# Performance work log

Hardware: AMD Instinct MI355X
Metric: run time of the kernel (lower is better)

Reference implementation:

```python
import jax, jax.numpy as jnp
import numpy as np
import math

B, S, D_MODEL, N_HEAD = 4, 2048, 1024, 16
D_K = D_MODEL // N_HEAD
ROPE_THETA = 10000.0


def _rope(x):
    # x: [B, H, S, Dk]; interleaved-pair rotary embedding.
    b, h, s, d = x.shape
    inv_freq = ROPE_THETA ** (-jnp.arange(0, d, 2, dtype=jnp.float32) / d)  # [d/2]
    ang = jnp.arange(s, dtype=jnp.float32)[:, None] * inv_freq[None, :]      # [S, d/2]
    cos, sin = jnp.cos(ang), jnp.sin(ang)
    x1, x2 = x[..., 0::2], x[..., 1::2]
    r1 = x1 * cos - x2 * sin
    r2 = x1 * sin + x2 * cos
    return jnp.stack([r1, r2], axis=-1).reshape(b, h, s, d)


def setup_inputs() -> dict:
    key = jax.random.key(0)
    ks = jax.random.split(key, 7)
    sc = 1.0 / math.sqrt(D_MODEL)
    return {
        "q": jax.random.normal(ks[0], (B, S, D_MODEL), jnp.float32),
        "k": jax.random.normal(ks[1], (B, S, D_MODEL), jnp.float32),
        "v": jax.random.normal(ks[2], (B, S, D_MODEL), jnp.float32),
        "Wq": jax.random.normal(ks[3], (D_MODEL, D_MODEL), jnp.float32) * sc,
        "Wk": jax.random.normal(ks[4], (D_MODEL, D_MODEL), jnp.float32) * sc,
        "Wv": jax.random.normal(ks[5], (D_MODEL, D_MODEL), jnp.float32) * sc,
        "Wo": jax.random.normal(ks[6], (D_MODEL, D_MODEL), jnp.float32) * sc,
    }


def _split(x):
    b, s, d = x.shape
    return x.reshape(b, s, N_HEAD, d // N_HEAD).transpose(0, 2, 1, 3)  # [B,H,S,Dk]


def reference(q, k, v, Wq, Wk, Wv, Wo):
    q = jnp.einsum("bsd,de->bse", q, Wq)
    k = jnp.einsum("bsd,de->bse", k, Wk)
    v = jnp.einsum("bsd,de->bse", v, Wv)
    qh, kh, vh = _split(q), _split(k), _split(v)
    qh, kh = _rope(qh), _rope(kh)
    scale = 1.0 / math.sqrt(D_K)
    score = jnp.einsum("bhqd,bhkd->bhqk", qh, kh) * scale  # [B,H,S,S]
    attn = jax.nn.softmax(score, axis=-1)
    out = jnp.einsum("bhqk,bhkd->bhqd", attn, vh)
    out = out.transpose(0, 2, 1, 3).reshape(q.shape[0], q.shape[1], D_MODEL)
    return jnp.einsum("bsd,de->bse", out, Wo)
```

## Files before the change

kernel.cpp:

```cpp
#include <hip/hip_runtime.h>
#include <stdint.h>

#define Bv 4
#define Sv 2048
#define Dv 1024
#define Hv 16
#define DKv 64
#define BSv (Bv * Sv)

typedef unsigned short u16;
typedef __attribute__((ext_vector_type(8))) short short8;
typedef __attribute__((ext_vector_type(8))) unsigned short u16x8;
typedef __attribute__((ext_vector_type(4))) unsigned short u16x4;
typedef __attribute__((ext_vector_type(4))) float f32x4;

__device__ __forceinline__ u16 f2bf(float f) {
  union { float f; uint32_t u; } x; x.f = f;
  uint32_t r = x.u + 0x7FFFu + ((x.u >> 16) & 1u);
  return (u16)(r >> 16);
}

__device__ __forceinline__ void gl_lds16(const void* g, void* l) {
  __builtin_amdgcn_global_load_lds(
      (__attribute__((address_space(1))) void*)g,
      (__attribute__((address_space(3))) void*)l, 16, 0, 0);
}

__device__ __forceinline__ f32x4 mfma16(short8 a, short8 b, f32x4 c) {
  return __builtin_amdgcn_mfma_f32_16x16x32_bf16(a, b, c, 0, 0, 0);
}

__global__ __launch_bounds__(256) void conv_qkv(
    const float* __restrict__ q, const float* __restrict__ k,
    const float* __restrict__ v, u16* __restrict__ qb, u16* __restrict__ kb,
    u16* __restrict__ vb) {
  const float* src = (blockIdx.y == 0) ? q : (blockIdx.y == 1 ? k : v);
  u16* dst = (blockIdx.y == 0) ? qb : (blockIdx.y == 1 ? kb : vb);
  int i = (blockIdx.x * 256 + threadIdx.x) * 8;
  const float4* s4 = (const float4*)(src + i);
  float4 a = s4[0], b = s4[1];
  u16x8 o = { f2bf(a.x), f2bf(a.y), f2bf(a.z), f2bf(a.w),
              f2bf(b.x), f2bf(b.y), f2bf(b.z), f2bf(b.w) };
  *(u16x8*)(dst + i) = o;
}

__global__ __launch_bounds__(256) void conv_wt(
    const float* __restrict__ w0, const float* __restrict__ w1,
    const float* __restrict__ w2, const float* __restrict__ w3,
    u16* __restrict__ t0, u16* __restrict__ t1, u16* __restrict__ t2,
    u16* __restrict__ t3) {
  const float* W = (blockIdx.z == 0) ? w0 : (blockIdx.z == 1 ? w1 : (blockIdx.z == 2 ? w2 : w3));
  u16* T = (blockIdx.z == 0) ? t0 : (blockIdx.z == 1 ? t1 : (blockIdx.z == 2 ? t2 : t3));
  __shared__ u16 tile[64][72];
  int nb = blockIdx.x * 64, kb = blockIdx.y * 64;
  int t = threadIdx.x;
#pragma unroll
  for (int p = 0; p < 4; ++p) {
    int idx = p * 256 + t;
    int r = idx >> 4;
    int c4 = (idx & 15) * 4;
    float4 vv = *(const float4*)(W + (size_t)(kb + r) * Dv + nb + c4);
    tile[c4 + 0][r] = f2bf(vv.x);
    tile[c4 + 1][r] = f2bf(vv.y);
    tile[c4 + 2][r] = f2bf(vv.z);
    tile[c4 + 3][r] = f2bf(vv.w);
  }
  __syncthreads();
#pragma unroll
  for (int p = 0; p < 4; ++p) {
    int idx = p * 256 + t;
    int r = idx >> 4;
    int c4 = (idx & 15) * 4;
    u16x4 o = { tile[r][c4], tile[r][c4 + 1], tile[r][c4 + 2], tile[r][c4 + 3] };
    *(u16x4*)(T + (size_t)(nb + r) * Dv + kb + c4) = o;
  }
}

__global__ __launch_bounds__(256) void gemm_bt(
    const u16* __restrict__ A, const u16* __restrict__ Bt,
    void* __restrict__ Out, int mode) {
  __shared__ u16 As[128 * 64];
  __shared__ u16 Bs[128 * 64];
  int tid = threadIdx.x;
  int lane = tid & 63, wid = tid >> 6;
  int quad = lane >> 4, cc = lane & 15;
  int wm = (wid >> 1) * 64, wn = (wid & 1) * 64;
  int m0 = blockIdx.x * 128, n0 = blockIdx.y * 128;

  f32x4 acc[4][4];
#pragma unroll
  for (int mi = 0; mi < 4; ++mi)
#pragma unroll
    for (int ni = 0; ni < 4; ++ni) {
      f32x4 z = {0.f, 0.f, 0.f, 0.f};
      acc[mi][ni] = z;
    }

  for (int k0 = 0; k0 < Dv; k0 += 64) {
#pragma unroll
    for (int p = 0; p < 4; ++p) {
      int slot = p * 256 + tid;
      int row = slot >> 3, cl = slot & 7;
      int cg = cl ^ (row & 7);
      gl_lds16(A + (size_t)(m0 + row) * Dv + k0 + cg * 8, &As[slot * 8]);
    }
#pragma unroll
    for (int p = 0; p < 4; ++p) {
      int slot = p * 256 + tid;
      int row = slot >> 3, cl = slot & 7;
      int cg = cl ^ (row & 7);
      gl_lds16(Bt + (size_t)(n0 + row) * Dv + k0 + cg * 8, &Bs[slot * 8]);
    }
    __syncthreads();
#pragma unroll
    for (int kk = 0; kk < 2; ++kk) {
      short8 af[4], bf[4];
#pragma unroll
      for (int mi = 0; mi < 4; ++mi) {
        int row = wm + mi * 16 + cc;
        int cg = kk * 4 + quad;
        af[mi] = *(const short8*)&As[row * 64 + (cg ^ (row & 7)) * 8];
      }
#pragma unroll
      for (int ni = 0; ni < 4; ++ni) {
        int row = wn + ni * 16 + cc;
        int cg = kk * 4 + quad;
        bf[ni] = *(const short8*)&Bs[row * 64 + (cg ^ (row & 7)) * 8];
      }
#pragma unroll
      for (int mi = 0; mi < 4; ++mi)
#pragma unroll
        for (int ni = 0; ni < 4; ++ni)
          acc[mi][ni] = mfma16(af[mi], bf[ni], acc[mi][ni]);
    }
    __syncthreads();
  }

  if (mode <= 1) {
    u16* O = (u16*)Out;
    float postscale = (mode == 0) ? 0.125f : 1.0f;
#pragma unroll
    for (int ni = 0; ni < 4; ++ni) {
      int n = n0 + wn + ni * 16 + cc;
      int h = n >> 6, d = n & 63;
      float inv = __expf(-(float)(d & 62) * (9.210340372f / 64.0f));
      float sign = (d & 1) ? 1.0f : -1.0f;
#pragma unroll
      for (int mi = 0; mi < 4; ++mi) {
        int mB = m0 + wm + mi * 16 + quad * 4;
#pragma unroll
        for (int r = 0; r < 4; ++r) {
          int m = mB + r;
          int b = m >> 11, s = m & (Sv - 1);
          float val = acc[mi][ni][r];
          float part = __shfl_xor(val, 1);
          float sn, cs;
          __sincosf((float)s * inv, &sn, &cs);
          float outv = (val * cs + sign * part * sn) * postscale;
          O[((size_t)(b * Hv + h) * Sv + s) * DKv + d] = f2bf(outv);
        }
      }
    }
  } else if (mode == 2) {
    u16* O = (u16*)Out;
#pragma unroll
    for (int ni = 0; ni < 4; ++ni) {
      int n = n0 + wn + ni * 16 + cc;
      int h = n >> 6, d = n & 63;
#pragma unroll
      for (int mi = 0; mi < 4; ++mi) {
        int mB = m0 + wm + mi * 16 + quad * 4;
        int b = mB >> 11, s = mB & (Sv - 1);
        u16x4 o4 = { f2bf(acc[mi][ni][0]), f2bf(acc[mi][ni][1]),
                     f2bf(acc[mi][ni][2]), f2bf(acc[mi][ni][3]) };
        *(u16x4*)&O[((size_t)(b * Hv + h) * DKv + d) * Sv + s] = o4;
      }
    }
  } else {
    float* O = (float*)Out;
#pragma unroll
    for (int ni = 0; ni < 4; ++ni) {
      int n = n0 + wn + ni * 16 + cc;
#pragma unroll
      for (int mi = 0; mi < 4; ++mi) {
        int mB = m0 + wm + mi * 16 + quad * 4;
#pragma unroll
        for (int r = 0; r < 4; ++r)
          O[(size_t)(mB + r) * Dv + n] = acc[mi][ni][r];
      }
    }
  }
}

__global__ __launch_bounds__(256) void attn(
    const u16* __restrict__ Qp, const u16* __restrict__ Kp,
    const u16* __restrict__ Vt, u16* __restrict__ ctx) {
  __shared__ u16 Ks[2][64 * 64];
  __shared__ u16 Vs[2][64 * 64];
  __shared__ u16 Ps[4][32 * 72];
  int tid = threadIdx.x;
  int lane = tid & 63, wid = tid >> 6;
  int quad = lane >> 4, cc = lane & 15;
  int bh = blockIdx.y;
  int q0 = blockIdx.x * 128 + wid * 32;
  const u16* Qh = Qp + (size_t)bh * Sv * DKv;
  const u16* Kh = Kp + (size_t)bh * Sv * DKv;
  const u16* Vh = Vt + (size_t)bh * Sv * DKv;

  short8 qf[2][2];
#pragma unroll
  for (int mi = 0; mi < 2; ++mi)
#pragma unroll
    for (int kk = 0; kk < 2; ++kk)
      qf[mi][kk] = *(const short8*)&Qh[(size_t)(q0 + mi * 16 + cc) * DKv + kk * 32 + quad * 8];

  f32x4 o[2][4];
  float lacc[2][4];
#pragma unroll
  for (int mi = 0; mi < 2; ++mi) {
#pragma unroll
    for (int nd = 0; nd < 4; ++nd) {
      f32x4 z = {0.f, 0.f, 0.f, 0.f};
      o[mi][nd] = z;
    }
#pragma unroll
    for (int r = 0; r < 4; ++r) lacc[mi][r] = 0.f;
  }

#pragma unroll
  for (int p = 0; p < 2; ++p) {
    int slot = p * 256 + tid;
    int row = slot >> 3, cl = slot & 7;
    int cg = cl ^ (row & 7);
    gl_lds16(Kh + (size_t)row * DKv + cg * 8, &Ks[0][slot * 8]);
    gl_lds16(Vh + (size_t)row * Sv + cg * 8, &Vs[0][slot * 8]);
  }

  for (int kt = 0; kt < Sv / 64; ++kt) {
    int cur = kt & 1;
    __syncthreads();

    if (kt + 1 < Sv / 64) {
      int s1 = (kt + 1) * 64;
#pragma unroll
      for (int p = 0; p < 2; ++p) {
        int slot = p * 256 + tid;
        int row = slot >> 3, cl = slot & 7;
        int cg = cl ^ (row & 7);
        gl_lds16(Kh + (size_t)(s1 + row) * DKv + cg * 8, &Ks[1 - cur][slot * 8]);
        gl_lds16(Vh + (size_t)row * Sv + s1 + cg * 8, &Vs[1 - cur][slot * 8]);
      }
    }

    f32x4 sc[2][4];
#pragma unroll
    for (int mi = 0; mi < 2; ++mi)
#pragma unroll
      for (int kc = 0; kc < 4; ++kc) {
        f32x4 z = {0.f, 0.f, 0.f, 0.f};
        sc[mi][kc] = z;
      }
#pragma unroll
    for (int kk = 0; kk < 2; ++kk) {
      short8 kf[4];
#pragma unroll
      for (int kc = 0; kc < 4; ++kc) {
        int row = kc * 16 + cc;
        int cg = kk * 4 + quad;
        kf[kc] = *(const short8*)&Ks[cur][row * 64 + (cg ^ (row & 7)) * 8];
      }
#pragma unroll
      for (int mi = 0; mi < 2; ++mi)
#pragma unroll
        for (int kc = 0; kc < 4; ++kc)
          sc[mi][kc] = mfma16(qf[mi][kk], kf[kc], sc[mi][kc]);
    }

#pragma unroll
    for (int mi = 0; mi < 2; ++mi)
#pragma unroll
      for (int kc = 0; kc < 4; ++kc)
#pragma unroll
        for (int r = 0; r < 4; ++r) {
          float pv = __expf(sc[mi][kc][r]);
          uint32_t u = __float_as_uint(pv);
          lacc[mi][r] += __uint_as_float(u & 0xFFFF0000u);
          Ps[wid][(mi * 16 + quad * 4 + r) * 72 + kc * 16 + cc] = (u16)(u >> 16);
        }

#pragma unroll
    for (int kk = 0; kk < 2; ++kk) {
      short8 pf[2], vf[4];
#pragma unroll
      for (int mi = 0; mi < 2; ++mi)
        pf[mi] = *(const short8*)&Ps[wid][(mi * 16 + cc) * 72 + (kk * 4 + quad) * 8];
#pragma unroll
      for (int nd = 0; nd < 4; ++nd) {
        int row = nd * 16 + cc;
        int cg = kk * 4 + quad;
        vf[nd] = *(const short8*)&Vs[cur][row * 64 + (cg ^ (row & 7)) * 8];
      }
#pragma unroll
      for (int mi = 0; mi < 2; ++mi)
#pragma unroll
        for (int nd = 0; nd < 4; ++nd)
          o[mi][nd] = mfma16(pf[mi], vf[nd], o[mi][nd]);
    }
  }

#pragma unroll
  for (int mi = 0; mi < 2; ++mi)
#pragma unroll
    for (int r = 0; r < 4; ++r) {
      float l = lacc[mi][r];
#pragma unroll
      for (int off = 1; off < 16; off <<= 1)
        l += __shfl_xor(l, off);
      lacc[mi][r] = 1.0f / l;
    }

  int b = bh >> 4, h = bh & 15;
#pragma unroll
  for (int mi = 0; mi < 2; ++mi)
#pragma unroll
    for (int r = 0; r < 4; ++r) {
      int s = q0 + mi * 16 + quad * 4 + r;
      float linv = lacc[mi][r];
#pragma unroll
      for (int nd = 0; nd < 4; ++nd) {
        int d = h * DKv + nd * 16 + cc;
        ctx[((size_t)b * Sv + s) * Dv + d] = f2bf(o[mi][nd][r] * linv);
      }
    }
}

extern "C" void kernel_launch(void* const* d_in, const int* in_sizes, int n_in,
                              void* d_out, int out_size, void* d_ws, size_t ws_size,
                              hipStream_t stream) {
  (void)in_sizes; (void)n_in; (void)out_size; (void)ws_size;
  const float* q  = (const float*)d_in[0];
  const float* k  = (const float*)d_in[1];
  const float* v  = (const float*)d_in[2];
  const float* Wq = (const float*)d_in[3];
  const float* Wk = (const float*)d_in[4];
  const float* Wv = (const float*)d_in[5];
  const float* Wo = (const float*)d_in[6];

  char* ws = (char*)d_ws;
  size_t off = 0;
  const size_t big = (size_t)BSv * Dv * sizeof(u16);
  const size_t wsz = (size_t)Dv * Dv * sizeof(u16);
  u16* qb  = (u16*)(ws + off); off += big;
  u16* kb  = (u16*)(ws + off); off += big;
  u16* vb  = (u16*)(ws + off); off += big;
  u16* Wqt = (u16*)(ws + off); off += wsz;
  u16* Wkt = (u16*)(ws + off); off += wsz;
  u16* Wvt = (u16*)(ws + off); off += wsz;
  u16* Wot = (u16*)(ws + off); off += wsz;
  u16* Qp  = (u16*)(ws + off); off += big;
  u16* Kp  = (u16*)(ws + off); off += big;
  u16* Vtr = (u16*)(ws + off); off += big;
  u16* ctx = (u16*)(ws + off); off += big;

  conv_qkv<<<dim3(BSv * Dv / (256 * 8), 3), 256, 0, stream>>>(q, k, v, qb, kb, vb);
  conv_wt<<<dim3(Dv / 64, Dv / 64, 4), 256, 0, stream>>>(Wq, Wk, Wv, Wo, Wqt, Wkt, Wvt, Wot);
  gemm_bt<<<dim3(BSv / 128, Dv / 128), 256, 0, stream>>>(qb, Wqt, Qp, 0);
  gemm_bt<<<dim3(BSv / 128, Dv / 128), 256, 0, stream>>>(kb, Wkt, Kp, 1);
  gemm_bt<<<dim3(BSv / 128, Dv / 128), 256, 0, stream>>>(vb, Wvt, Vtr, 2);
  attn<<<dim3(Sv / 128, Bv * Hv), 256, 0, stream>>>(Qp, Kp, Vtr, ctx);
  gemm_bt<<<dim3(BSv / 128, Dv / 128), 256, 0, stream>>>(ctx, Wot, d_out, 3);
}
```

Baseline: 371.1 us.

## Double attention query tile per wave, use exp2 and MFMA row-sum

```diff
diff --git a/kernel.cpp b/kernel.cpp
--- a/kernel.cpp
+++ b/kernel.cpp
@@ -138,7 +138,7 @@
 
   if (mode <= 1) {
     u16* O = (u16*)Out;
-    float postscale = (mode == 0) ? 0.125f : 1.0f;
+    float postscale = (mode == 0) ? 0.18033688011112042f : 1.0f;
 #pragma unroll
     for (int ni = 0; ni < 4; ++ni) {
       int n = n0 + wn + ni * 16 + cc;
@@ -197,34 +197,37 @@
     const u16* __restrict__ Vt, u16* __restrict__ ctx) {
   __shared__ u16 Ks[2][64 * 64];
   __shared__ u16 Vs[2][64 * 64];
-  __shared__ u16 Ps[4][32 * 72];
+  __shared__ u16 Ps[4][64 * 72];
   int tid = threadIdx.x;
   int lane = tid & 63, wid = tid >> 6;
   int quad = lane >> 4, cc = lane & 15;
   int bh = blockIdx.y;
-  int q0 = blockIdx.x * 128 + wid * 32;
+  int q0 = blockIdx.x * 256 + wid * 64;
   const u16* Qh = Qp + (size_t)bh * Sv * DKv;
   const u16* Kh = Kp + (size_t)bh * Sv * DKv;
   const u16* Vh = Vt + (size_t)bh * Sv * DKv;
 
-  short8 qf[2][2];
-#pragma unroll
-  for (int mi = 0; mi < 2; ++mi)
+  const short8 ones = { (short)0x3F80, (short)0x3F80, (short)0x3F80, (short)0x3F80,
+                        (short)0x3F80, (short)0x3F80, (short)0x3F80, (short)0x3F80 };
+
+  short8 qf[4][2];
+#pragma unroll
+  for (int mi = 0; mi < 4; ++mi)
 #pragma unroll
     for (int kk = 0; kk < 2; ++kk)
       qf[mi][kk] = *(const short8*)&Qh[(size_t)(q0 + mi * 16 + cc) * DKv + kk * 32 + quad * 8];
 
-  f32x4 o[2][4];
-  float lacc[2][4];
-#pragma unroll
-  for (int mi = 0; mi < 2; ++mi) {
+  f32x4 o[4][4];
+  f32x4 ol[4];
+#pragma unroll
+  for (int mi = 0; mi < 4; ++mi) {
 #pragma unroll
     for (int nd = 0; nd < 4; ++nd) {
       f32x4 z = {0.f, 0.f, 0.f, 0.f};
       o[mi][nd] = z;
     }
-#pragma unroll
-    for (int r = 0; r < 4; ++r) lacc[mi][r] = 0.f;
+    f32x4 z = {0.f, 0.f, 0.f, 0.f};
+    ol[mi] = z;
   }
 
 #pragma unroll
@@ -252,48 +255,42 @@
       }
     }
 
-    f32x4 sc[2][4];
-#pragma unroll
-    for (int mi = 0; mi < 2; ++mi)
+    short8 kf[4][2];
+#pragma unroll
+    for (int kc = 0; kc < 4; ++kc)
+#pragma unroll
+      for (int kk = 0; kk < 2; ++kk) {
+        int row = kc * 16 + cc;
+        int cg = kk * 4 + quad;
+        kf[kc][kk] = *(const short8*)&Ks[cur][row * 64 + (cg ^ (row & 7)) * 8];
+      }
+
+#pragma unroll
+    for (int mi = 0; mi < 4; ++mi) {
+      f32x4 sc[4];
 #pragma unroll
       for (int kc = 0; kc < 4; ++kc) {
         f32x4 z = {0.f, 0.f, 0.f, 0.f};
-        sc[mi][kc] = z;
-      }
+        sc[kc] = z;
+      }
+#pragma unroll
+      for (int kk = 0; kk < 2; ++kk)
+#pragma unroll
+        for (int kc = 0; kc < 4; ++kc)
+          sc[kc] = mfma16(qf[mi][kk], kf[kc][kk], sc[kc]);
+#pragma unroll
+      for (int kc = 0; kc < 4; ++kc)
+#pragma unroll
+        for (int r = 0; r < 4; ++r) {
+          float pv = __builtin_amdgcn_exp2f(sc[kc][r]);
+          Ps[wid][(mi * 16 + quad * 4 + r) * 72 + kc * 16 + cc] =
+              (u16)(__float_as_uint(pv) >> 16);
+        }
+    }
+
 #pragma unroll
     for (int kk = 0; kk < 2; ++kk) {
-      short8 kf[4];
-#pragma unroll
-      for (int kc = 0; kc < 4; ++kc) {
-        int row = kc * 16 + cc;
-        int cg = kk * 4 + quad;
-        kf[kc] = *(const short8*)&Ks[cur][row * 64 + (cg ^ (row & 7)) * 8];
-      }
-#pragma unroll
-      for (int mi = 0; mi < 2; ++mi)
-#pragma unroll
-        for (int kc = 0; kc < 4; ++kc)
-          sc[mi][kc] = mfma16(qf[mi][kk], kf[kc], sc[mi][kc]);
-    }
-
-#pragma unroll
-    for (int mi = 0; mi < 2; ++mi)
-#pragma unroll
-      for (int kc = 0; kc < 4; ++kc)
-#pragma unroll
-        for (int r = 0; r < 4; ++r) {
-          float pv = __expf(sc[mi][kc][r]);
-          uint32_t u = __float_as_uint(pv);
-          lacc[mi][r] += __uint_as_float(u & 0xFFFF0000u);
-          Ps[wid][(mi * 16 + quad * 4 + r) * 72 + kc * 16 + cc] = (u16)(u >> 16);
-        }
-
-#pragma unroll
-    for (int kk = 0; kk < 2; ++kk) {
-      short8 pf[2], vf[4];
-#pragma unroll
-      for (int mi = 0; mi < 2; ++mi)
-        pf[mi] = *(const short8*)&Ps[wid][(mi * 16 + cc) * 72 + (kk * 4 + quad) * 8];
+      short8 vf[4], pf[4];
 #pragma unroll
       for (int nd = 0; nd < 4; ++nd) {
         int row = nd * 16 + cc;
@@ -301,31 +298,26 @@
         vf[nd] = *(const short8*)&Vs[cur][row * 64 + (cg ^ (row & 7)) * 8];
       }
 #pragma unroll
-      for (int mi = 0; mi < 2; ++mi)
+      for (int mi = 0; mi < 4; ++mi)
+        pf[mi] = *(const short8*)&Ps[wid][(mi * 16 + cc) * 72 + (kk * 4 + quad) * 8];
+#pragma unroll
+      for (int mi = 0; mi < 4; ++mi)
+        ol[mi] = mfma16(pf[mi], ones, ol[mi]);
+#pragma unroll
+      for (int mi = 0; mi < 4; ++mi)
 #pragma unroll
         for (int nd = 0; nd < 4; ++nd)
           o[mi][nd] = mfma16(pf[mi], vf[nd], o[mi][nd]);
     }
   }
 
-#pragma unroll
-  for (int mi = 0; mi < 2; ++mi)
-#pragma unroll
-    for (int r = 0; r < 4; ++r) {
-      float l = lacc[mi][r];
-#pragma unroll
-      for (int off = 1; off < 16; off <<= 1)
-        l += __shfl_xor(l, off);
-      lacc[mi][r] = 1.0f / l;
-    }
-
   int b = bh >> 4, h = bh & 15;
 #pragma unroll
-  for (int mi = 0; mi < 2; ++mi)
+  for (int mi = 0; mi < 4; ++mi)
 #pragma unroll
     for (int r = 0; r < 4; ++r) {
       int s = q0 + mi * 16 + quad * 4 + r;
-      float linv = lacc[mi][r];
+      float linv = 1.0f / ol[mi][r];
 #pragma unroll
       for (int nd = 0; nd < 4; ++nd) {
         int d = h * DKv + nd * 16 + cc;
@@ -367,6 +359,6 @@
   gemm_bt<<<dim3(BSv / 128, Dv / 128), 256, 0, stream>>>(qb, Wqt, Qp, 0);
   gemm_bt<<<dim3(BSv / 128, Dv / 128), 256, 0, stream>>>(kb, Wkt, Kp, 1);
   gemm_bt<<<dim3(BSv / 128, Dv / 128), 256, 0, stream>>>(vb, Wvt, Vtr, 2);
-  attn<<<dim3(Sv / 128, Bv * Hv), 256, 0, stream>>>(Qp, Kp, Vtr, ctx);
+  attn<<<dim3(Sv / 256, Bv * Hv), 256, 0, stream>>>(Qp, Kp, Vtr, ctx);
   gemm_bt<<<dim3(BSv / 128, Dv / 128), 256, 0, stream>>>(ctx, Wot, d_out, 3);
 }
```

Result: slower. 392.6 us (+5.8%).
